# Performance work log

Hardware: AMD Instinct MI355X
Metric: run time of the kernel (lower is better)

## Reference

```python
import jax, jax.numpy as jnp
import numpy as np

D_MODEL = 256
D_INNER = 512      # expand(2) * d_model
D_STATE = 16
DT_RANK = 16       # ceil(256/16)
D_CONV = 4
DEPTH = 2


def _silu(x):
    return x * jax.nn.sigmoid(x)


def _selective_scan(u, dt, A, B, C, D):
    # u,dt: [b,l,d]; A: [d,n]; B,C: [b,l,n]; D: [d]
    dA = jnp.einsum('bld,dn->bldn', dt, A)
    dBu = jnp.einsum('bld,bld,bln->bldn', dt, u, B)
    # torch: F.pad(dA[:,1:], last-l-dim one zero).flip(1).cumsum(1).exp().flip(1)
    dA_shift = jnp.concatenate([dA[:, 1:], jnp.zeros_like(dA[:, :1])], axis=1)
    dAc = jnp.exp(jnp.cumsum(dA_shift[:, ::-1], axis=1)[:, ::-1])
    x = jnp.cumsum(dBu * dAc, axis=1) / (dAc + 1e-12)
    y = jnp.einsum('bldn,bln->bld', x, C)
    return y + u * D


def _block(x, p):
    # x: [b,l,d_model]
    in_w, conv_w, conv_b, xproj_w, dt_w, dt_b, A_log, Dp, out_w = p
    xr = jnp.einsum('bld,ed->ble', x, in_w)           # [b,l,2*d_inner]
    xx, res = jnp.split(xr, 2, axis=-1)
    # causal depthwise conv1d (padding d_conv-1 then truncate == left-pad)
    xc = jax.lax.conv_general_dilated(
        xx.transpose(0, 2, 1), conv_w, window_strides=(1,),
        padding=[(D_CONV - 1, 0)], feature_group_count=D_INNER,
        dimension_numbers=('NCH', 'OIH', 'NCH')) + conv_b[None, :, None]
    xx = _silu(xc.transpose(0, 2, 1))                 # [b,l,d_inner]
    x_dbl = jnp.einsum('bld,ed->ble', xx, xproj_w)
    delta = x_dbl[..., :DT_RANK]
    B = x_dbl[..., DT_RANK:DT_RANK + D_STATE]
    C = x_dbl[..., DT_RANK + D_STATE:]
    delta = jax.nn.softplus(jnp.einsum('blr,dr->bld', delta, dt_w) + dt_b)
    A = -jnp.exp(A_log)
    y = _selective_scan(xx, delta, A, B, C, Dp)
    y = y * _silu(res)
    return jnp.einsum('bld,od->blo', y, out_w)


def _model1(x, params):
    for i in range(DEPTH):
        x = _block(x, tuple(q[i] for q in params))
    return x


def setup_inputs() -> dict:
    key = jax.random.key(0)
    ks = jax.random.split(key, 8)

    def nrm(k, shape, scale):
        return (jax.random.normal(k, shape) * scale).astype(jnp.float32)

    x0 = jax.random.normal(ks[0], (4, D_MODEL, 256, 256), jnp.float32)
    in_w = nrm(ks[1], (DEPTH, 2 * D_INNER, D_MODEL), 0.02)
    conv_w = nrm(ks[2], (DEPTH, D_INNER, 1, D_CONV), 0.1)
    conv_b = jnp.zeros((DEPTH, D_INNER), jnp.float32)
    xproj_w = nrm(ks[3], (DEPTH, DT_RANK + 2 * D_STATE, D_INNER), 0.02)
    dt_w = nrm(ks[4], (DEPTH, D_INNER, DT_RANK), 0.05)
    dt_b = jnp.full((DEPTH, D_INNER), -4.0, jnp.float32)  # small deltas for stability
    A_log = jnp.tile(jnp.log(jnp.arange(1, D_STATE + 1, dtype=jnp.float32))[None, None, :],
                     (DEPTH, D_INNER, 1))
    Dp = jnp.ones((DEPTH, D_INNER), jnp.float32)
    out_w = nrm(ks[5], (DEPTH, D_MODEL, D_INNER), 0.02)
    return dict(x0=x0, in_w=in_w, conv_w=conv_w, conv_b=conv_b, xproj_w=xproj_w,
                dt_w=dt_w, dt_b=dt_b, A_log=A_log, Dp=Dp, out_w=out_w)


def reference(x0, in_w, conv_w, conv_b, xproj_w, dt_w, dt_b, A_log, Dp, out_w):
    params = (in_w, conv_w, conv_b, xproj_w, dt_w, dt_b, A_log, Dp, out_w)
    # h-axis: pool over w, mamba over length h (weights shared with w pass)
    x_h = x0.mean(axis=3)                                        # [b,c,h]
    xm_h = _model1(x_h.transpose(0, 2, 1), params)               # [b,h,c]
    xm_h = xm_h.transpose(0, 2, 1)[..., None] * x0               # [b,c,h,w]
    # w-axis: pool over h of gated map, mamba over length w
    x_w = xm_h.mean(axis=2)                                      # [b,c,w]
    xm_w = _model1(x_w.transpose(0, 2, 1), params)               # [b,w,c]
    return xm_w.transpose(0, 2, 1)[:, :, None, :] * x0           # [b,c,h,w]
```

## Files before the change

kernel.cpp:

```cpp
#include <hip/hip_runtime.h>
#include <math.h>

#define BSZ 4
#define DM 256
#define LL 256
#define DI 512
#define NBL (BSZ * LL)

__global__ void k_nop() {}

__global__ __launch_bounds__(256) void k_meanw_prep(const float* __restrict__ x0,
                                                    const float* __restrict__ in_w1,
                                                    const float* __restrict__ out_w0,
                                                    float* __restrict__ S0,
                                                    float* __restrict__ Wf) {
    __shared__ float smem[1664];
    int bl = blockIdx.x;
    int tid = threadIdx.x;
    if (bl < 1024) {
        int wv = tid >> 6, lane = tid & 63;
        const float4* x4 = (const float4*)x0;
        int rbase = bl * 256 + wv * 64;
        for (int i0 = 0; i0 < 64; i0 += 4) {
            float s[4];
#pragma unroll
            for (int j = 0; j < 4; ++j) {
                float4 v = x4[(size_t)(rbase + i0 + j) * 64 + lane];
                s[j] = (v.x + v.y) + (v.z + v.w);
            }
#pragma unroll
            for (int j = 0; j < 4; ++j) {
#pragma unroll
                for (int m = 32; m >= 1; m >>= 1) s[j] += __shfl_xor(s[j], m);
            }
            if (lane == 0) {
#pragma unroll
                for (int j = 0; j < 4; ++j) {
                    int rr = rbase + i0 + j;
                    int b = rr >> 16, d = (rr >> 8) & 255, h = rr & 255;
                    S0[((size_t)(b * LL) + h) * DM + d] = s[j] * (1.0f / 256.0f);
                }
            }
        }
    } else {
        float* As = smem;
        float* Bs = smem + 576;
        int t = bl - 1024;
        int e0 = (t >> 4) * 32, k0c = (t & 15) * 32;
        int tx = tid & 15, ty = tid >> 4;
        float acc00 = 0.f, acc01 = 0.f, acc10 = 0.f, acc11 = 0.f;
        for (int dm0 = 0; dm0 < 256; dm0 += 16) {
            float4 v;
            if (tid < 128) {
                int r = tid >> 2, q = tid & 3;
                v = *(const float4*)(in_w1 + (size_t)(e0 + r) * 256 + dm0 + 4 * q);
            } else {
                int idx = tid - 128;
                int r = idx >> 3, q = idx & 7;
                v = *(const float4*)(out_w0 + (size_t)(dm0 + r) * 512 + k0c + 4 * q);
            }
            __syncthreads();
            if (tid < 128) {
                int r = tid >> 2, q = tid & 3;
                As[(4 * q + 0) * 36 + r] = v.x;
                As[(4 * q + 1) * 36 + r] = v.y;
                As[(4 * q + 2) * 36 + r] = v.z;
                As[(4 * q + 3) * 36 + r] = v.w;
            } else {
                int idx = tid - 128;
                int r = idx >> 3, q = idx & 7;
                Bs[r * 36 + 4 * q + 0] = v.x;
                Bs[r * 36 + 4 * q + 1] = v.y;
                Bs[r * 36 + 4 * q + 2] = v.z;
                Bs[r * 36 + 4 * q + 3] = v.w;
            }
            __syncthreads();
#pragma unroll
            for (int kk = 0; kk < 16; ++kk) {
                float2 a = *(const float2*)(As + kk * 36 + 2 * ty);
                float2 b = *(const float2*)(Bs + kk * 36 + 2 * tx);
                acc00 = fmaf(a.x, b.x, acc00);
                acc01 = fmaf(a.x, b.y, acc01);
                acc10 = fmaf(a.y, b.x, acc10);
                acc11 = fmaf(a.y, b.y, acc11);
            }
        }
        float* c0 = Wf + (size_t)(e0 + 2 * ty) * 512 + k0c + 2 * tx;
        c0[0] = acc00; c0[1] = acc01;
        c0[512] = acc10; c0[513] = acc11;
    }
}

__global__ __launch_bounds__(256) void k_gemm_nt32(const float* __restrict__ A,
                                                   const float* __restrict__ Bw,
                                                   float* __restrict__ C,
                                                   int M, int N, int K) {
    __shared__ float As[16][36];
    __shared__ float Bs[16][68];
    int tid = threadIdx.x;
    int tx = tid & 15, ty = tid >> 4;
    int n0 = blockIdx.x * 64;
    int m0 = blockIdx.y * 32;
    int lr = tid >> 2;
    int lk = (tid & 3) * 4;

    float acc[2][4];
#pragma unroll
    for (int i = 0; i < 2; ++i)
#pragma unroll
        for (int j = 0; j < 4; ++j) acc[i][j] = 0.0f;

    for (int k0 = 0; k0 < K; k0 += 16) {
        float4 bv = *(const float4*)(Bw + (size_t)(n0 + lr) * K + k0 + lk);
        float4 av;
        if (tid < 128) av = *(const float4*)(A + (size_t)(m0 + lr) * K + k0 + lk);
        __syncthreads();
        Bs[lk + 0][lr] = bv.x; Bs[lk + 1][lr] = bv.y; Bs[lk + 2][lr] = bv.z; Bs[lk + 3][lr] = bv.w;
        if (tid < 128) {
            As[lk + 0][lr] = av.x; As[lk + 1][lr] = av.y; As[lk + 2][lr] = av.z; As[lk + 3][lr] = av.w;
        }
        __syncthreads();
#pragma unroll
        for (int kk = 0; kk < 16; ++kk) {
            float2 a = *(const float2*)(&As[kk][2 * ty]);
            float4 bf = *(const float4*)(&Bs[kk][4 * tx]);
            acc[0][0] = fmaf(a.x, bf.x, acc[0][0]);
            acc[0][1] = fmaf(a.x, bf.y, acc[0][1]);
            acc[0][2] = fmaf(a.x, bf.z, acc[0][2]);
            acc[0][3] = fmaf(a.x, bf.w, acc[0][3]);
            acc[1][0] = fmaf(a.y, bf.x, acc[1][0]);
            acc[1][1] = fmaf(a.y, bf.y, acc[1][1]);
            acc[1][2] = fmaf(a.y, bf.z, acc[1][2]);
            acc[1][3] = fmaf(a.y, bf.w, acc[1][3]);
        }
    }
#pragma unroll
    for (int i = 0; i < 2; ++i) {
        float4 o;
        o.x = acc[i][0]; o.y = acc[i][1]; o.z = acc[i][2]; o.w = acc[i][3];
        *(float4*)(C + (size_t)(m0 + 2 * ty + i) * N + n0 + 4 * tx) = o;
    }
}

__global__ __launch_bounds__(256) void k_gemm_tn(const float* __restrict__ At,
                                                 const float* __restrict__ B,
                                                 float* __restrict__ C,
                                                 int ldc) {
    __shared__ float As[16 * 36];
    __shared__ float Bs[16 * 68];
    int tid = threadIdx.x;
    int tx = tid & 15, ty = tid >> 4;
    int n0 = blockIdx.x * 64;
    int m0 = blockIdx.y * 32;
    int b = m0 >> 8, l0 = m0 & 255;

    float acc[2][4];
#pragma unroll
    for (int i = 0; i < 2; ++i)
#pragma unroll
        for (int j = 0; j < 4; ++j) acc[i][j] = 0.0f;

    for (int d0 = 0; d0 < 512; d0 += 16) {
        float4 va, vb1, vb2;
        if (tid < 128) {
            int r = tid >> 3, q = tid & 7;
            va = *(const float4*)(At + ((size_t)(b * 512 + d0 + r)) * 256 + l0 + 4 * q);
        } else {
            int idx = tid - 128;
            int nr = idx >> 1, q = idx & 1;
            const float* bp = B + (size_t)(n0 + nr) * 512 + d0 + 8 * q;
            vb1 = *(const float4*)(bp);
            vb2 = *(const float4*)(bp + 4);
        }
        __syncthreads();
        if (tid < 128) {
            int r = tid >> 3, q = tid & 7;
            *(float4*)(As + r * 36 + 4 * q) = va;
        } else {
            int idx = tid - 128, nr = idx >> 1, q = idx & 1;
            Bs[(8 * q + 0) * 68 + nr] = vb1.x;
            Bs[(8 * q + 1) * 68 + nr] = vb1.y;
            Bs[(8 * q + 2) * 68 + nr] = vb1.z;
            Bs[(8 * q + 3) * 68 + nr] = vb1.w;
            Bs[(8 * q + 4) * 68 + nr] = vb2.x;
            Bs[(8 * q + 5) * 68 + nr] = vb2.y;
            Bs[(8 * q + 6) * 68 + nr] = vb2.z;
            Bs[(8 * q + 7) * 68 + nr] = vb2.w;
        }
        __syncthreads();
#pragma unroll
        for (int kk = 0; kk < 16; ++kk) {
            float2 a = *(const float2*)(As + kk * 36 + 2 * ty);
            float4 bf = *(const float4*)(Bs + kk * 68 + 4 * tx);
            acc[0][0] = fmaf(a.x, bf.x, acc[0][0]);
            acc[0][1] = fmaf(a.x, bf.y, acc[0][1]);
            acc[0][2] = fmaf(a.x, bf.z, acc[0][2]);
            acc[0][3] = fmaf(a.x, bf.w, acc[0][3]);
            acc[1][0] = fmaf(a.y, bf.x, acc[1][0]);
            acc[1][1] = fmaf(a.y, bf.y, acc[1][1]);
            acc[1][2] = fmaf(a.y, bf.z, acc[1][2]);
            acc[1][3] = fmaf(a.y, bf.w, acc[1][3]);
        }
    }
#pragma unroll
    for (int i = 0; i < 2; ++i) {
        float4 o;
        o.x = acc[i][0]; o.y = acc[i][1]; o.z = acc[i][2]; o.w = acc[i][3];
        *(float4*)(C + (size_t)(m0 + 2 * ty + i) * ldc + n0 + 4 * tx) = o;
    }
}

__global__ __launch_bounds__(256) void k_gemm_tn32(const float* __restrict__ At,
                                                   const float* __restrict__ B,
                                                   float* __restrict__ C,
                                                   int ldc) {
    __shared__ float As[16 * 36];
    __shared__ float Bs[16 * 36];
    int tid = threadIdx.x;
    int tx = tid & 15, ty = tid >> 4;
    int n0 = blockIdx.x * 32;
    int m0 = blockIdx.y * 32;
    int b = m0 >> 8, l0 = m0 & 255;

    float acc00 = 0.f, acc01 = 0.f, acc10 = 0.f, acc11 = 0.f;
    for (int d0 = 0; d0 < 512; d0 += 16) {
        float4 v;
        if (tid < 128) {
            int r = tid >> 3, q = tid & 7;
            v = *(const float4*)(At + ((size_t)(b * 512 + d0 + r)) * 256 + l0 + 4 * q);
        } else {
            int idx = tid - 128;
            int nr = idx >> 2, q = idx & 3;
            v = *(const float4*)(B + (size_t)(n0 + nr) * 512 + d0 + 4 * q);
        }
        __syncthreads();
        if (tid < 128) {
            int r = tid >> 3, q = tid & 7;
            *(float4*)(As + r * 36 + 4 * q) = v;
        } else {
            int idx = tid - 128;
            int nr = idx >> 2, q = idx & 3;
            Bs[(4 * q + 0) * 36 + nr] = v.x;
            Bs[(4 * q + 1) * 36 + nr] = v.y;
            Bs[(4 * q + 2) * 36 + nr] = v.z;
            Bs[(4 * q + 3) * 36 + nr] = v.w;
        }
        __syncthreads();
#pragma unroll
        for (int kk = 0; kk < 16; ++kk) {
            float2 a = *(const float2*)(As + kk * 36 + 2 * ty);
            float2 bb = *(const float2*)(Bs + kk * 36 + 2 * tx);
            acc00 = fmaf(a.x, bb.x, acc00);
            acc01 = fmaf(a.x, bb.y, acc01);
            acc10 = fmaf(a.y, bb.x, acc10);
            acc11 = fmaf(a.y, bb.y, acc11);
        }
    }
    float2 o0; o0.x = acc00; o0.y = acc01;
    float2 o1; o1.x = acc10; o1.y = acc11;
    *(float2*)(C + (size_t)(m0 + 2 * ty + 0) * ldc + n0 + 2 * tx) = o0;
    *(float2*)(C + (size_t)(m0 + 2 * ty + 1) * ldc + n0 + 2 * tx) = o1;
}

__global__ __launch_bounds__(256) void k_mid(const float* __restrict__ xz,
                                             const float* __restrict__ cw,
                                             const float* __restrict__ cb,
                                             const float* __restrict__ xpw,
                                             float* __restrict__ xx,
                                             float* __restrict__ xdbl) {
    __shared__ float xs[DI];
    __shared__ float pr[256];
    int bl = blockIdx.x;
    int b = bl >> 8, l = bl & 255;
    int tid = threadIdx.x;

#pragma unroll
    for (int c = 0; c < 2; ++c) {
        int d = tid + 256 * c;
        float4 w4 = *(const float4*)(cw + d * 4);
        float acc = cb[d];
#pragma unroll
        for (int k = 0; k < 4; ++k) {
            int ls = l + k - 3;
            float v = (ls >= 0) ? xz[((size_t)(b * LL + ls)) * 1024 + d] : 0.0f;
            acc = fmaf(((const float*)&w4)[k], v, acc);
        }
        float v = acc / (1.0f + expf(-acc));
        xs[d] = v;
        xx[(size_t)bl * DI + d] = v;
    }
    __syncthreads();

    int e = tid >> 2, c2 = tid & 3;
    float a = 0.0f;
    if (e < 48) {
        const float4* xv4 = (const float4*)(xs + c2 * 128);
        const float4* wv4 = (const float4*)(xpw + (size_t)e * DI + c2 * 128);
#pragma unroll 8
        for (int q = 0; q < 32; ++q) {
            float4 x4 = xv4[q], p4 = wv4[q];
            a = fmaf(x4.x, p4.x, a);
            a = fmaf(x4.y, p4.y, a);
            a = fmaf(x4.z, p4.z, a);
            a = fmaf(x4.w, p4.w, a);
        }
    }
    pr[tid] = a;
    __syncthreads();
    if (tid < 48)
        xdbl[(size_t)bl * 48 + tid] = pr[4 * tid] + pr[4 * tid + 1] + pr[4 * tid + 2] + pr[4 * tid + 3];
}

__global__ __launch_bounds__(256) void k_scan(const float* __restrict__ xx,
                                              const float* __restrict__ xdbl,
                                              const float* __restrict__ xz,
                                              const float* __restrict__ Alog,
                                              const float* __restrict__ Dp,
                                              const float* __restrict__ dtw,
                                              const float* __restrict__ dtb,
                                              float* __restrict__ ygT) {
    __shared__ float yred[4][LL];
    __shared__ float us[LL];
    int tid = threadIdx.x;
    int lane = tid & 63, w = tid >> 6;
    int seq = blockIdx.x;
    int d = seq & (DI - 1), b = seq >> 9;
    int l0 = lane * 4;

    const float* xd0 = xdbl + ((size_t)(b * LL) + l0) * 48;
    const float* wr = dtw + d * 16;
    float4 w0 = *(const float4*)(wr + 0);
    float4 w1 = *(const float4*)(wr + 4);
    float4 w2 = *(const float4*)(wr + 8);
    float4 w3 = *(const float4*)(wr + 12);
    float bias = dtb[d];

    float dt[4], u[4], dtu[4], P[4];
#pragma unroll
    for (int i = 0; i < 4; ++i) {
        const float* xr = xd0 + i * 48;
        float4 a0 = *(const float4*)(xr + 0);
        float4 a1 = *(const float4*)(xr + 4);
        float4 a2 = *(const float4*)(xr + 8);
        float4 a3 = *(const float4*)(xr + 12);
        float acc = bias;
        acc = fmaf(a0.x, w0.x, acc); acc = fmaf(a0.y, w0.y, acc);
        acc = fmaf(a0.z, w0.z, acc); acc = fmaf(a0.w, w0.w, acc);
        acc = fmaf(a1.x, w1.x, acc); acc = fmaf(a1.y, w1.y, acc);
        acc = fmaf(a1.z, w1.z, acc); acc = fmaf(a1.w, w1.w, acc);
        acc = fmaf(a2.x, w2.x, acc); acc = fmaf(a2.y, w2.y, acc);
        acc = fmaf(a2.z, w2.z, acc); acc = fmaf(a2.w, w2.w, acc);
        acc = fmaf(a3.x, w3.x, acc); acc = fmaf(a3.y, w3.y, acc);
        acc = fmaf(a3.z, w3.z, acc); acc = fmaf(a3.w, w3.w, acc);
        dt[i] = (acc > 20.0f) ? acc : log1pf(expf(acc));
        u[i] = xx[((size_t)(b * LL) + l0 + i) * DI + d];
        dtu[i] = dt[i] * u[i];
    }

    P[0] = dt[0]; P[1] = P[0] + dt[1]; P[2] = P[1] + dt[2]; P[3] = P[2] + dt[3];
    float s = P[3];
#pragma unroll
    for (int off = 1; off < 64; off <<= 1) {
        float t = __shfl_up(s, off);
        if (lane >= off) s += t;
    }
    float base = s - P[3];
    float dt_end = __shfl(s, 63);
    float Dtc[4];
#pragma unroll
    for (int i = 0; i < 4; ++i) Dtc[i] = P[i] + base;

    if (w == 0) {
#pragma unroll
        for (int i = 0; i < 4; ++i) us[l0 + i] = u[i];
    }

    float4 Al = *(const float4*)(Alog + d * 16 + 4 * w);
    float A[4] = {-expf(Al.x), -expf(Al.y), -expf(Al.z), -expf(Al.w)};
    float Bv[4][4], Cv[4][4];
#pragma unroll
    for (int i = 0; i < 4; ++i) {
        float4 bq = *(const float4*)(xd0 + i * 48 + 16 + 4 * w);
        float4 cq = *(const float4*)(xd0 + i * 48 + 32 + 4 * w);
        Bv[i][0] = bq.x; Bv[i][1] = bq.y; Bv[i][2] = bq.z; Bv[i][3] = bq.w;
        Cv[i][0] = cq.x; Cv[i][1] = cq.y; Cv[i][2] = cq.z; Cv[i][3] = cq.w;
    }

    float y[4] = {0.f, 0.f, 0.f, 0.f};
#pragma unroll
    for (int c = 0; c < 4; ++c) {
        float Ac = A[c];
        float dAc[4], t[4];
#pragma unroll
        for (int i = 0; i < 4; ++i) {
            dAc[i] = expf(Ac * (dt_end - Dtc[i]));
            t[i] = dtu[i] * Bv[i][c] * dAc[i];
        }
        float p0 = t[0], p1 = p0 + t[1], p2 = p1 + t[2], p3 = p2 + t[3];
        float ss = p3;
#pragma unroll
        for (int off = 1; off < 64; off <<= 1) {
            float tt = __shfl_up(ss, off);
            if (lane >= off) ss += tt;
        }
        float baseT = ss - p3;
        y[0] += (p0 + baseT) / (dAc[0] + 1e-12f) * Cv[0][c];
        y[1] += (p1 + baseT) / (dAc[1] + 1e-12f) * Cv[1][c];
        y[2] += (p2 + baseT) / (dAc[2] + 1e-12f) * Cv[2][c];
        y[3] += (p3 + baseT) / (dAc[3] + 1e-12f) * Cv[3][c];
    }
#pragma unroll
    for (int i = 0; i < 4; ++i) yred[w][l0 + i] = y[i];
    __syncthreads();

    int l = tid;
    float ysum = yred[0][l] + yred[1][l] + yred[2][l] + yred[3][l];
    float yv = fmaf(us[l], Dp[d], ysum);
    float res = xz[((size_t)(b * LL) + l) * 1024 + DI + d];
    ygT[(size_t)seq * LL + l] = yv * (res / (1.0f + expf(-res)));
}

__global__ __launch_bounds__(256) void k_fuse_mean_h(const float* __restrict__ m,
                                                     const float* __restrict__ x0,
                                                     float* __restrict__ xw) {
    int bd = blockIdx.x;
    int b = bd >> 8, d = bd & 255;
    int w = threadIdx.x;
    __shared__ float ms[LL];
    ms[w] = m[((size_t)(b * LL) + w) * DM + d];
    __syncthreads();
    const float* xrow = x0 + (size_t)bd * 65536;
    float a0 = 0.0f, a1 = 0.0f, a2 = 0.0f, a3 = 0.0f;
    for (int h = 0; h < 256; h += 8) {
        float xv[8];
#pragma unroll
        for (int j = 0; j < 8; ++j) xv[j] = xrow[(size_t)(h + j) * 256 + w];
        a0 = fmaf(ms[h + 0], xv[0], a0);
        a1 = fmaf(ms[h + 1], xv[1], a1);
        a2 = fmaf(ms[h + 2], xv[2], a2);
        a3 = fmaf(ms[h + 3], xv[3], a3);
        a0 = fmaf(ms[h + 4], xv[4], a0);
        a1 = fmaf(ms[h + 5], xv[5], a1);
        a2 = fmaf(ms[h + 6], xv[6], a2);
        a3 = fmaf(ms[h + 7], xv[7], a3);
    }
    float acc = (a0 + a1) + (a2 + a3);
    xw[((size_t)(b * LL) + w) * DM + d] = acc * (1.0f / 256.0f);
}

__global__ __launch_bounds__(256) void k_final(const float* __restrict__ mw,
                                               const float* __restrict__ x0,
                                               float* __restrict__ out) {
    __shared__ float ms[LL];
    int bd = blockIdx.x;
    int b = bd >> 8, d = bd & 255;
    int tid = threadIdx.x;
    ms[tid] = mw[((size_t)(b * LL) + tid) * DM + d];
    __syncthreads();

    int w4 = tid & 63;
    int hq = tid >> 6;
    float4 mv = *(const float4*)(ms + (w4 << 2));
    const float4* xin = (const float4*)(x0 + (size_t)bd * 65536);
    float4* oout = (float4*)(out + (size_t)bd * 65536);
#pragma unroll 4
    for (int hi = 0; hi < 64; ++hi) {
        int h = hi * 4 + hq;
        size_t idx = (size_t)h * 64 + w4;
        float4 xv = xin[idx];
        float4 o;
        o.x = mv.x * xv.x;
        o.y = mv.y * xv.y;
        o.z = mv.z * xv.z;
        o.w = mv.w * xv.w;
        oout[idx] = o;
    }
}

extern "C" void kernel_launch(void* const* d_in, const int* in_sizes, int n_in,
                              void* d_out, int out_size, void* d_ws, size_t ws_size,
                              hipStream_t stream) {
    const float* x0      = (const float*)d_in[0];
    const float* in_w    = (const float*)d_in[1];
    const float* conv_w  = (const float*)d_in[2];
    const float* conv_b  = (const float*)d_in[3];
    const float* xproj_w = (const float*)d_in[4];
    const float* dt_w    = (const float*)d_in[5];
    const float* dt_b    = (const float*)d_in[6];
    const float* A_log   = (const float*)d_in[7];
    const float* Dp      = (const float*)d_in[8];
    const float* out_w   = (const float*)d_in[9];
    float* out = (float*)d_out;

    float* S0   = (float*)d_ws;
    float* Sout = S0 + 262144;
    float* Wf   = Sout + 262144;
    float* xz   = Wf + 524288;
    float* xx   = xz + 1048576;
    float* xdbl = xx + 524288;
    float* ygT  = xdbl + 49152;

    const float* out_w1 = out_w + 131072;

    auto run_model = [&](const float* inb, float* outb) {
        k_gemm_nt32<<<dim3(16, 32), 256, 0, stream>>>(inb, in_w, xz, NBL, 1024, 256);
        k_mid<<<NBL, 256, 0, stream>>>(xz, conv_w, conv_b, xproj_w, xx, xdbl);
        k_scan<<<BSZ * DI, 256, 0, stream>>>(xx, xdbl, xz, A_log, Dp, dt_w, dt_b, ygT);
        k_gemm_tn<<<dim3(16, 32), 256, 0, stream>>>(ygT, Wf, xz, 1024);
        k_mid<<<NBL, 256, 0, stream>>>(xz, conv_w + 2048, conv_b + 512,
                                       xproj_w + 24576, xx, xdbl);
        k_scan<<<BSZ * DI, 256, 0, stream>>>(xx, xdbl, xz, A_log + 8192, Dp + 512,
                                             dt_w + 8192, dt_b + 512, ygT);
        k_gemm_tn32<<<dim3(8, 32), 256, 0, stream>>>(ygT, out_w1, outb, 256);
    };

    k_meanw_prep<<<1536, 256, 0, stream>>>(x0, in_w + 262144, out_w, S0, Wf);
    run_model(S0, Sout);
    k_fuse_mean_h<<<NBL, 256, 0, stream>>>(Sout, x0, S0);
    run_model(S0, Sout);
    k_final<<<NBL, 256, 0, stream>>>(Sout, x0, out);

    for (int i = 0; i < 16; ++i) k_nop<<<1, 64, 0, stream>>>();
}
```

Measured before the change: 571.6 us.

## Use 64x64 register-prefetched GEMM tiles, swizzle block order by batch, drop nop launches

```diff
diff --git a/kernel.cpp b/kernel.cpp
--- a/kernel.cpp
+++ b/kernel.cpp
@@ -7,7 +7,10 @@
 #define DI 512
 #define NBL (BSZ * LL)
 
-__global__ void k_nop() {}
+__device__ __forceinline__ void unswz(int j, int& b, int& i) {
+    b = (j & 7) >> 1;
+    i = ((j >> 3) << 1) | (j & 1);
+}
 
 __global__ __launch_bounds__(256) void k_meanw_prep(const float* __restrict__ x0,
                                                     const float* __restrict__ in_w1,
@@ -18,9 +21,11 @@
     int bl = blockIdx.x;
     int tid = threadIdx.x;
     if (bl < 1024) {
+        int b, i; unswz(bl, b, i);
+        int rowblk = (b << 8) | i;
         int wv = tid >> 6, lane = tid & 63;
         const float4* x4 = (const float4*)x0;
-        int rbase = bl * 256 + wv * 64;
+        int rbase = rowblk * 256 + wv * 64;
         for (int i0 = 0; i0 < 64; i0 += 4) {
             float s[4];
 #pragma unroll
@@ -37,8 +42,8 @@
 #pragma unroll
                 for (int j = 0; j < 4; ++j) {
                     int rr = rbase + i0 + j;
-                    int b = rr >> 16, d = (rr >> 8) & 255, h = rr & 255;
-                    S0[((size_t)(b * LL) + h) * DM + d] = s[j] * (1.0f / 256.0f);
+                    int bb = rr >> 16, d = (rr >> 8) & 255, h = rr & 255;
+                    S0[((size_t)(bb * LL) + h) * DM + d] = s[j] * (1.0f / 256.0f);
                 }
             }
         }
@@ -78,11 +83,11 @@
 #pragma unroll
             for (int kk = 0; kk < 16; ++kk) {
                 float2 a = *(const float2*)(As + kk * 36 + 2 * ty);
-                float2 b = *(const float2*)(Bs + kk * 36 + 2 * tx);
-                acc00 = fmaf(a.x, b.x, acc00);
-                acc01 = fmaf(a.x, b.y, acc01);
-                acc10 = fmaf(a.y, b.x, acc10);
-                acc11 = fmaf(a.y, b.y, acc11);
+                float2 b2 = *(const float2*)(Bs + kk * 36 + 2 * tx);
+                acc00 = fmaf(a.x, b2.x, acc00);
+                acc01 = fmaf(a.x, b2.y, acc01);
+                acc10 = fmaf(a.y, b2.x, acc10);
+                acc11 = fmaf(a.y, b2.y, acc11);
             }
         }
         float* c0 = Wf + (size_t)(e0 + 2 * ty) * 512 + k0c + 2 * tx;
@@ -91,136 +96,125 @@
     }
 }
 
-__global__ __launch_bounds__(256) void k_gemm_nt32(const float* __restrict__ A,
+__global__ __launch_bounds__(256) void k_gemm_nt64(const float* __restrict__ A,
                                                    const float* __restrict__ Bw,
-                                                   float* __restrict__ C,
-                                                   int M, int N, int K) {
-    __shared__ float As[16][36];
+                                                   float* __restrict__ C) {
+    __shared__ float As[16][68];
     __shared__ float Bs[16][68];
     int tid = threadIdx.x;
+    int b, i; unswz(blockIdx.x, b, i);
+    int m0 = b * 256 + (i >> 4) * 64;
+    int n0 = (i & 15) * 64;
     int tx = tid & 15, ty = tid >> 4;
-    int n0 = blockIdx.x * 64;
-    int m0 = blockIdx.y * 32;
-    int lr = tid >> 2;
-    int lk = (tid & 3) * 4;
-
-    float acc[2][4];
-#pragma unroll
-    for (int i = 0; i < 2; ++i)
-#pragma unroll
-        for (int j = 0; j < 4; ++j) acc[i][j] = 0.0f;
-
-    for (int k0 = 0; k0 < K; k0 += 16) {
-        float4 bv = *(const float4*)(Bw + (size_t)(n0 + lr) * K + k0 + lk);
-        float4 av;
-        if (tid < 128) av = *(const float4*)(A + (size_t)(m0 + lr) * K + k0 + lk);
+    int r = tid >> 2, kq = (tid & 3) * 4;
+
+    const float* pa = A + (size_t)(m0 + r) * 256 + kq;
+    const float* pb = Bw + (size_t)(n0 + r) * 256 + kq;
+    float4 ra = *(const float4*)pa;
+    float4 rb = *(const float4*)pb;
+
+    float acc[4][4];
+#pragma unroll
+    for (int ii = 0; ii < 4; ++ii)
+#pragma unroll
+        for (int jj = 0; jj < 4; ++jj) acc[ii][jj] = 0.0f;
+
+    for (int k0 = 0; k0 < 256; k0 += 16) {
         __syncthreads();
-        Bs[lk + 0][lr] = bv.x; Bs[lk + 1][lr] = bv.y; Bs[lk + 2][lr] = bv.z; Bs[lk + 3][lr] = bv.w;
-        if (tid < 128) {
-            As[lk + 0][lr] = av.x; As[lk + 1][lr] = av.y; As[lk + 2][lr] = av.z; As[lk + 3][lr] = av.w;
-        }
+        As[kq + 0][r] = ra.x; As[kq + 1][r] = ra.y; As[kq + 2][r] = ra.z; As[kq + 3][r] = ra.w;
+        Bs[kq + 0][r] = rb.x; Bs[kq + 1][r] = rb.y; Bs[kq + 2][r] = rb.z; Bs[kq + 3][r] = rb.w;
         __syncthreads();
+        if (k0 + 16 < 256) {
+            ra = *(const float4*)(pa + k0 + 16);
+            rb = *(const float4*)(pb + k0 + 16);
+        }
 #pragma unroll
         for (int kk = 0; kk < 16; ++kk) {
-            float2 a = *(const float2*)(&As[kk][2 * ty]);
-            float4 bf = *(const float4*)(&Bs[kk][4 * tx]);
-            acc[0][0] = fmaf(a.x, bf.x, acc[0][0]);
-            acc[0][1] = fmaf(a.x, bf.y, acc[0][1]);
-            acc[0][2] = fmaf(a.x, bf.z, acc[0][2]);
-            acc[0][3] = fmaf(a.x, bf.w, acc[0][3]);
-            acc[1][0] = fmaf(a.y, bf.x, acc[1][0]);
-            acc[1][1] = fmaf(a.y, bf.y, acc[1][1]);
-            acc[1][2] = fmaf(a.y, bf.z, acc[1][2]);
-            acc[1][3] = fmaf(a.y, bf.w, acc[1][3]);
-        }
-    }
-#pragma unroll
-    for (int i = 0; i < 2; ++i) {
+            float4 a4 = *(const float4*)(&As[kk][ty * 4]);
+            float4 b4 = *(const float4*)(&Bs[kk][tx * 4]);
+            float aa[4] = {a4.x, a4.y, a4.z, a4.w};
+            float bb[4] = {b4.x, b4.y, b4.z, b4.w};
+#pragma unroll
+            for (int ii = 0; ii < 4; ++ii)
+#pragma unroll
+                for (int jj = 0; jj < 4; ++jj)
+                    acc[ii][jj] = fmaf(aa[ii], bb[jj], acc[ii][jj]);
+        }
+    }
+#pragma unroll
+    for (int ii = 0; ii < 4; ++ii) {
         float4 o;
-        o.x = acc[i][0]; o.y = acc[i][1]; o.z = acc[i][2]; o.w = acc[i][3];
-        *(float4*)(C + (size_t)(m0 + 2 * ty + i) * N + n0 + 4 * tx) = o;
-    }
-}
-
-__global__ __launch_bounds__(256) void k_gemm_tn(const float* __restrict__ At,
-                                                 const float* __restrict__ B,
-                                                 float* __restrict__ C,
-                                                 int ldc) {
-    __shared__ float As[16 * 36];
-    __shared__ float Bs[16 * 68];
-    int tid = threadIdx.x;
+        o.x = acc[ii][0]; o.y = acc[ii][1]; o.z = acc[ii][2]; o.w = acc[ii][3];
+        *(float4*)(C + (size_t)(m0 + ty * 4 + ii) * 1024 + n0 + tx * 4) = o;
+    }
+}
+
+__global__ __launch_bounds__(256) void k_gemm_tn64(const float* __restrict__ At,
+                                                   const float* __restrict__ Bw,
+                                                   float* __restrict__ C) {
+    __shared__ float As[16][68];
+    __shared__ float Bs[16][68];
+    int tid = threadIdx.x;
+    int b, i; unswz(blockIdx.x, b, i);
+    int l0 = (i >> 4) * 64;
+    int n0 = (i & 15) * 64;
+    int m0 = b * 256 + l0;
     int tx = tid & 15, ty = tid >> 4;
-    int n0 = blockIdx.x * 64;
-    int m0 = blockIdx.y * 32;
-    int b = m0 >> 8, l0 = m0 & 255;
-
-    float acc[2][4];
-#pragma unroll
-    for (int i = 0; i < 2; ++i)
-#pragma unroll
-        for (int j = 0; j < 4; ++j) acc[i][j] = 0.0f;
+    int rkk = tid >> 4, mq = (tid & 15) * 4;
+    int rn = tid >> 2, dq = (tid & 3) * 4;
+
+    const float* pa = At + ((size_t)(b * 512) + rkk) * 256 + l0 + mq;
+    const float* pb = Bw + (size_t)(n0 + rn) * 512 + dq;
+    float4 ra = *(const float4*)pa;
+    float4 rb = *(const float4*)pb;
+
+    float acc[4][4];
+#pragma unroll
+    for (int ii = 0; ii < 4; ++ii)
+#pragma unroll
+        for (int jj = 0; jj < 4; ++jj) acc[ii][jj] = 0.0f;
 
     for (int d0 = 0; d0 < 512; d0 += 16) {
-        float4 va, vb1, vb2;
-        if (tid < 128) {
-            int r = tid >> 3, q = tid & 7;
-            va = *(const float4*)(At + ((size_t)(b * 512 + d0 + r)) * 256 + l0 + 4 * q);
-        } else {
-            int idx = tid - 128;
-            int nr = idx >> 1, q = idx & 1;
-            const float* bp = B + (size_t)(n0 + nr) * 512 + d0 + 8 * q;
-            vb1 = *(const float4*)(bp);
-            vb2 = *(const float4*)(bp + 4);
-        }
         __syncthreads();
-        if (tid < 128) {
-            int r = tid >> 3, q = tid & 7;
-            *(float4*)(As + r * 36 + 4 * q) = va;
-        } else {
-            int idx = tid - 128, nr = idx >> 1, q = idx & 1;
-            Bs[(8 * q + 0) * 68 + nr] = vb1.x;
-            Bs[(8 * q + 1) * 68 + nr] = vb1.y;
-            Bs[(8 * q + 2) * 68 + nr] = vb1.z;
-            Bs[(8 * q + 3) * 68 + nr] = vb1.w;
-            Bs[(8 * q + 4) * 68 + nr] = vb2.x;
-            Bs[(8 * q + 5) * 68 + nr] = vb2.y;
-            Bs[(8 * q + 6) * 68 + nr] = vb2.z;
-            Bs[(8 * q + 7) * 68 + nr] = vb2.w;
-        }
+        *(float4*)(&As[rkk][mq]) = ra;
+        Bs[dq + 0][rn] = rb.x; Bs[dq + 1][rn] = rb.y; Bs[dq + 2][rn] = rb.z; Bs[dq + 3][rn] = rb.w;
         __syncthreads();
+        if (d0 + 16 < 512) {
+            ra = *(const float4*)(pa + (size_t)(d0 + 16) * 256);
+            rb = *(const float4*)(pb + d0 + 16);
+        }
 #pragma unroll
         for (int kk = 0; kk < 16; ++kk) {
-            float2 a = *(const float2*)(As + kk * 36 + 2 * ty);
-            float4 bf = *(const float4*)(Bs + kk * 68 + 4 * tx);
-            acc[0][0] = fmaf(a.x, bf.x, acc[0][0]);
-            acc[0][1] = fmaf(a.x, bf.y, acc[0][1]);
-            acc[0][2] = fmaf(a.x, bf.z, acc[0][2]);
-            acc[0][3] = fmaf(a.x, bf.w, acc[0][3]);
-            acc[1][0] = fmaf(a.y, bf.x, acc[1][0]);
-            acc[1][1] = fmaf(a.y, bf.y, acc[1][1]);
-            acc[1][2] = fmaf(a.y, bf.z, acc[1][2]);
-            acc[1][3] = fmaf(a.y, bf.w, acc[1][3]);
-        }
-    }
-#pragma unroll
-    for (int i = 0; i < 2; ++i) {
+            float4 a4 = *(const float4*)(&As[kk][ty * 4]);
+            float4 b4 = *(const float4*)(&Bs[kk][tx * 4]);
+            float aa[4] = {a4.x, a4.y, a4.z, a4.w};
+            float bb[4] = {b4.x, b4.y, b4.z, b4.w};
+#pragma unroll
+            for (int ii = 0; ii < 4; ++ii)
+#pragma unroll
+                for (int jj = 0; jj < 4; ++jj)
+                    acc[ii][jj] = fmaf(aa[ii], bb[jj], acc[ii][jj]);
+        }
+    }
+#pragma unroll
+    for (int ii = 0; ii < 4; ++ii) {
         float4 o;
-        o.x = acc[i][0]; o.y = acc[i][1]; o.z = acc[i][2]; o.w = acc[i][3];
-        *(float4*)(C + (size_t)(m0 + 2 * ty + i) * ldc + n0 + 4 * tx) = o;
+        o.x = acc[ii][0]; o.y = acc[ii][1]; o.z = acc[ii][2]; o.w = acc[ii][3];
+        *(float4*)(C + (size_t)(m0 + ty * 4 + ii) * 1024 + n0 + tx * 4) = o;
     }
 }
 
 __global__ __launch_bounds__(256) void k_gemm_tn32(const float* __restrict__ At,
                                                    const float* __restrict__ B,
-                                                   float* __restrict__ C,
-                                                   int ldc) {
+                                                   float* __restrict__ C) {
     __shared__ float As[16 * 36];
     __shared__ float Bs[16 * 36];
     int tid = threadIdx.x;
     int tx = tid & 15, ty = tid >> 4;
-    int n0 = blockIdx.x * 32;
-    int m0 = blockIdx.y * 32;
-    int b = m0 >> 8, l0 = m0 & 255;
+    int b, i; unswz(blockIdx.x, b, i);
+    int l0 = (i >> 3) * 32;
+    int n0 = (i & 7) * 32;
+    int m0 = b * 256 + l0;
 
     float acc00 = 0.f, acc01 = 0.f, acc10 = 0.f, acc11 = 0.f;
     for (int d0 = 0; d0 < 512; d0 += 16) {
@@ -258,8 +252,8 @@
     }
     float2 o0; o0.x = acc00; o0.y = acc01;
     float2 o1; o1.x = acc10; o1.y = acc11;
-    *(float2*)(C + (size_t)(m0 + 2 * ty + 0) * ldc + n0 + 2 * tx) = o0;
-    *(float2*)(C + (size_t)(m0 + 2 * ty + 1) * ldc + n0 + 2 * tx) = o1;
+    *(float2*)(C + (size_t)(m0 + 2 * ty + 0) * 256 + n0 + 2 * tx) = o0;
+    *(float2*)(C + (size_t)(m0 + 2 * ty + 1) * 256 + n0 + 2 * tx) = o1;
 }
 
 __global__ __launch_bounds__(256) void k_mid(const float* __restrict__ xz,
@@ -270,8 +264,8 @@
                                              float* __restrict__ xdbl) {
     __shared__ float xs[DI];
     __shared__ float pr[256];
-    int bl = blockIdx.x;
-    int b = bl >> 8, l = bl & 255;
+    int b, l; unswz(blockIdx.x, b, l);
+    int bl = (b << 8) | l;
     int tid = threadIdx.x;
 
 #pragma unroll
@@ -323,8 +317,8 @@
     __shared__ float us[LL];
     int tid = threadIdx.x;
     int lane = tid & 63, w = tid >> 6;
-    int seq = blockIdx.x;
-    int d = seq & (DI - 1), b = seq >> 9;
+    int b, d; unswz(blockIdx.x, b, d);
+    int seq = b * DI + d;
     int l0 = lane * 4;
 
     const float* xd0 = xdbl + ((size_t)(b * LL) + l0) * 48;
@@ -423,8 +417,8 @@
 __global__ __launch_bounds__(256) void k_fuse_mean_h(const float* __restrict__ m,
                                                      const float* __restrict__ x0,
                                                      float* __restrict__ xw) {
-    int bd = blockIdx.x;
-    int b = bd >> 8, d = bd & 255;
+    int b, d; unswz(blockIdx.x, b, d);
+    int bd = (b << 8) | d;
     int w = threadIdx.x;
     __shared__ float ms[LL];
     ms[w] = m[((size_t)(b * LL) + w) * DM + d];
@@ -452,8 +446,8 @@
                                                const float* __restrict__ x0,
                                                float* __restrict__ out) {
     __shared__ float ms[LL];
-    int bd = blockIdx.x;
-    int b = bd >> 8, d = bd & 255;
+    int b, d; unswz(blockIdx.x, b, d);
+    int bd = (b << 8) | d;
     int tid = threadIdx.x;
     ms[tid] = mw[((size_t)(b * LL) + tid) * DM + d];
     __syncthreads();
@@ -503,15 +497,15 @@
     const float* out_w1 = out_w + 131072;
 
     auto run_model = [&](const float* inb, float* outb) {
-        k_gemm_nt32<<<dim3(16, 32), 256, 0, stream>>>(inb, in_w, xz, NBL, 1024, 256);
+        k_gemm_nt64<<<256, 256, 0, stream>>>(inb, in_w, xz);
         k_mid<<<NBL, 256, 0, stream>>>(xz, conv_w, conv_b, xproj_w, xx, xdbl);
         k_scan<<<BSZ * DI, 256, 0, stream>>>(xx, xdbl, xz, A_log, Dp, dt_w, dt_b, ygT);
-        k_gemm_tn<<<dim3(16, 32), 256, 0, stream>>>(ygT, Wf, xz, 1024);
+        k_gemm_tn64<<<256, 256, 0, stream>>>(ygT, Wf, xz);
         k_mid<<<NBL, 256, 0, stream>>>(xz, conv_w + 2048, conv_b + 512,
                                        xproj_w + 24576, xx, xdbl);
         k_scan<<<BSZ * DI, 256, 0, stream>>>(xx, xdbl, xz, A_log + 8192, Dp + 512,
                                              dt_w + 8192, dt_b + 512, ygT);
-        k_gemm_tn32<<<dim3(8, 32), 256, 0, stream>>>(ygT, out_w1, outb, 256);
+        k_gemm_tn32<<<256, 256, 0, stream>>>(ygT, out_w1, outb);
     };
 
     k_meanw_prep<<<1536, 256, 0, stream>>>(x0, in_w + 262144, out_w, S0, Wf);
@@ -519,6 +513,4 @@
     k_fuse_mean_h<<<NBL, 256, 0, stream>>>(Sout, x0, S0);
     run_model(S0, Sout);
     k_final<<<NBL, 256, 0, stream>>>(Sout, x0, out);
-
-    for (int i = 0; i < 16; ++i) k_nop<<<1, 64, 0, stream>>>();
-}
+}
```

Result: faster. 508.4 us (-11.0%).
